# Kernel tuning notes

Measured on AMD Instinct MI355X. Metric: run time of the kernel, lower is better.

The kernel has to match this reference:

```python
import jax, jax.numpy as jnp
import numpy as np

N = 50000
E = 400000
H1, H2, D = 4, 2, 64
NEG_SLOPE = 0.2
EPS = 1e-5


def _segment_softmax(alpha, dst, num_nodes):
    # alpha: [E, H], softmax over edges sharing the same dst node
    m = jax.ops.segment_max(alpha, dst, num_segments=num_nodes)  # [N, H]
    ex = jnp.exp(alpha - m[dst])
    den = jax.ops.segment_sum(ex, dst, num_segments=num_nodes)   # [N, H]
    return ex / den[dst]


def _gat_conv(x, src, dst, eattr, W, We, a_src, a_dst, a_edge, b, heads, num_nodes):
    # x: [N, Fin] -> h: [N, H, D]; eattr: [E, Fe] -> e: [E, H, D]
    h = (x @ W).reshape(num_nodes, heads, D)
    e = (eattr @ We).reshape(-1, heads, D)
    al_src = jnp.einsum('nhd,hd->nh', h, a_src)   # [N, H]
    al_dst = jnp.einsum('nhd,hd->nh', h, a_dst)   # [N, H]
    al_e = jnp.einsum('ehd,hd->eh', e, a_edge)    # [E, H]
    alpha = al_src[src] + al_dst[dst] + al_e
    alpha = jax.nn.leaky_relu(alpha, NEG_SLOPE)
    alpha = _segment_softmax(alpha, dst, num_nodes)
    msg = h[src] * alpha[:, :, None]              # [E, H, D]
    out = jax.ops.segment_sum(msg, dst, num_segments=num_nodes)
    return out.reshape(num_nodes, heads * D) + b


def _graph_norm(x, w, b, mean_scale):
    # PyG GraphNorm over the whole (single) graph
    mean = jnp.mean(x, axis=0, keepdims=True)
    out = x - mean * mean_scale
    var = jnp.mean(out * out, axis=0, keepdims=True)
    return w * out / jnp.sqrt(var + EPS) + b


def _forward(x, edge_index, edge_attr,
             W1, We1, as1, ad1, ae1, b1, gn1_w, gn1_b, gn1_ms,
             W2, We2, as2, ad2, ae2, b2, gn2_w, gn2_b, gn2_ms,
             Wc, bc):
    # add self loops (PyG default), self-loop edge_attr = mean of edge_attr
    loops = jnp.arange(N)
    src = jnp.concatenate([edge_index[0], loops])
    dst = jnp.concatenate([edge_index[1], loops])
    ea_mean = jnp.mean(edge_attr, axis=0, keepdims=True)
    eattr = jnp.concatenate([edge_attr, jnp.broadcast_to(ea_mean, (N, edge_attr.shape[1]))])

    h = _gat_conv(x, src, dst, eattr, W1, We1, as1, ad1, ae1, b1, H1, N)
    h = jax.nn.elu(_graph_norm(h, gn1_w, gn1_b, gn1_ms))
    h = _gat_conv(h, src, dst, eattr, W2, We2, as2, ad2, ae2, b2, H2, N)
    h = jax.nn.elu(_graph_norm(h, gn2_w, gn2_b, gn2_ms))
    return h @ Wc + bc


def setup_inputs() -> dict:
    key = jax.random.key(0)
    ks = jax.random.split(key, 20)
    g = lambda k, shape, fan: jax.random.normal(k, shape, jnp.float32) * (1.0 / np.sqrt(fan))
    inp = {
        'x': jax.random.normal(ks[0], (N, 3), jnp.float32),
        'edge_index': jax.random.randint(ks[1], (2, E), 0, N),
        'edge_attr': jax.random.uniform(ks[2], (E, 2), jnp.float32),
        'W1': g(ks[3], (3, H1 * D), 3),
        'We1': g(ks[4], (2, H1 * D), 2),
        'as1': g(ks[5], (H1, D), D),
        'ad1': g(ks[6], (H1, D), D),
        'ae1': g(ks[7], (H1, D), D),
        'b1': jnp.zeros((H1 * D,), jnp.float32),
        'gn1_w': jnp.ones((H1 * D,), jnp.float32),
        'gn1_b': jnp.zeros((H1 * D,), jnp.float32),
        'gn1_ms': jnp.ones((H1 * D,), jnp.float32),
        'W2': g(ks[8], (H1 * D, H2 * D), H1 * D),
        'We2': g(ks[9], (2, H2 * D), 2),
        'as2': g(ks[10], (H2, D), D),
        'ad2': g(ks[11], (H2, D), D),
        'ae2': g(ks[12], (H2, D), D),
        'b2': jnp.zeros((H2 * D,), jnp.float32),
        'gn2_w': jnp.ones((H2 * D,), jnp.float32),
        'gn2_b': jnp.zeros((H2 * D,), jnp.float32),
        'gn2_ms': jnp.ones((H2 * D,), jnp.float32),
        # classifier 128 -> 13
        'Wc': g(ks[13], (H2 * D, 13), H2 * D),
        'bc': jnp.zeros((13,), jnp.float32),
    }
    return inp


def reference(x, edge_index, edge_attr,
              W1, We1, as1, ad1, ae1, b1, gn1_w, gn1_b, gn1_ms,
              W2, We2, as2, ad2, ae2, b2, gn2_w, gn2_b, gn2_ms,
              Wc, bc):
    return _forward(x, edge_index, edge_attr,
                    W1, We1, as1, ad1, ae1, b1, gn1_w, gn1_b, gn1_ms,
                    W2, We2, as2, ad2, ae2, b2, gn2_w, gn2_b, gn2_ms,
                    Wc, bc)
```

## Files before the change

### kernel.cpp

```cpp
#include <hip/hip_runtime.h>
#include <math.h>

#define NEG_SLOPE 0.2f
#define GEPS 1e-5f

typedef __attribute__((ext_vector_type(8))) short short8;
typedef __attribute__((ext_vector_type(4))) float floatx4;

__device__ __forceinline__ float wave_reduce_sum(float v) {
#pragma unroll
    for (int o = 32; o > 0; o >>= 1) v += __shfl_down(v, o);
    return v;
}

__device__ __forceinline__ ushort f2bf(float f) {
    union { float f; unsigned int i; } c;
    c.f = f;
    unsigned int b = c.i;
    b += 0x7fffu + ((b >> 16) & 1u);
    return (ushort)(b >> 16);
}

__device__ __forceinline__ float bf2f(ushort u) {
    union { unsigned int i; float f; } c;
    c.i = (unsigned int)u << 16;
    return c.f;
}

__device__ __forceinline__ float2 unpack_bf2(unsigned int u) {
    union { unsigned int i; float f; } a, b;
    a.i = u << 16;
    b.i = u & 0xffff0000u;
    return make_float2(a.f, b.f);
}

__device__ __forceinline__ unsigned int pack_bf2(float lo, float hi) {
    return (unsigned int)f2bf(lo) | ((unsigned int)f2bf(hi) << 16);
}

__device__ __forceinline__ float lrelu(float v) {
    return (v > 0.f) ? v : v * NEG_SLOPE;
}

__device__ __forceinline__ float elu_fast(float v) {
    return (v > 0.f) ? v : (__expf(v) - 1.f);
}

__global__ __launch_bounds__(256) void k_pre(
    const float* __restrict__ W1, const float* __restrict__ as1, const float* __restrict__ ad1,
    const float* __restrict__ ea, const int* __restrict__ dst,
    const float* __restrict__ W2, const float* __restrict__ We1,
    const float* __restrict__ ae1, const float* __restrict__ We2,
    const float* __restrict__ ae2,
    float* __restrict__ ea_sum, int* __restrict__ deg, uint4* __restrict__ Bfrag,
    float* __restrict__ C1, float* __restrict__ C2, float* __restrict__ Ps,
    float* __restrict__ Pd, int E) {
    int b = blockIdx.x;
    if (b < 16) {
        int t = b * 256 + threadIdx.x;
        int c = t >> 9, kk = (t >> 6) & 7, L = t & 63;
        int q = L >> 4, n = c * 16 + (L & 15);
        int k0 = kk * 32 + q * 8;
        unsigned int u0 = pack_bf2(W2[(k0 + 0) * 128 + n], W2[(k0 + 1) * 128 + n]);
        unsigned int u1 = pack_bf2(W2[(k0 + 2) * 128 + n], W2[(k0 + 3) * 128 + n]);
        unsigned int u2 = pack_bf2(W2[(k0 + 4) * 128 + n], W2[(k0 + 5) * 128 + n]);
        unsigned int u3 = pack_bf2(W2[(k0 + 6) * 128 + n], W2[(k0 + 7) * 128 + n]);
        Bfrag[t] = make_uint4(u0, u1, u2, u3);
        return;
    }
    if (b == 16) {
        int t = threadIdx.x, h = t >> 6, lane = t & 63;
        float p0 = We1[t] * ae1[t];
        float p1 = We1[256 + t] * ae1[t];
        p0 = wave_reduce_sum(p0);
        p1 = wave_reduce_sum(p1);
        if (lane == 0) { C1[h] = p0; C1[4 + h] = p1; }
        float av = as1[t], dv = ad1[t];
#pragma unroll
        for (int k = 0; k < 3; ++k) {
            float wv = W1[k * 256 + t];
            float ps = wave_reduce_sum(wv * av);
            float pd = wave_reduce_sum(wv * dv);
            if (lane == 0) { Ps[h * 3 + k] = ps; Pd[h * 3 + k] = pd; }
        }
        if (t < 128) {
            float q0 = We2[t] * ae2[t];
            float q1 = We2[128 + t] * ae2[t];
            q0 = wave_reduce_sum(q0);
            q1 = wave_reduce_sum(q1);
            if (lane == 0) { C2[h] = q0; C2[2 + h] = q1; }
        }
        return;
    }
    b -= 17;
    const float2* ea2 = (const float2*)ea;
    float s0 = 0.f, s1 = 0.f;
    for (int e = b * 256 + threadIdx.x; e < E; e += 256 * 256) {
        float2 v = ea2[e];
        s0 += v.x; s1 += v.y;
        atomicAdd(&deg[dst[e]], 1);
    }
    s0 = wave_reduce_sum(s0);
    s1 = wave_reduce_sum(s1);
    if ((threadIdx.x & 63) == 0) {
        atomicAdd(&ea_sum[0], s0);
        atomicAdd(&ea_sum[1], s1);
    }
}

__global__ void k_scan1(const int* __restrict__ deg, int* __restrict__ row_ptr,
                        int* __restrict__ bsum, int N) {
    __shared__ int tmp[1024];
    int tid = threadIdx.x;
    int i = blockIdx.x * 1024 + tid;
    int v = (i < N) ? deg[i] : 0;
    tmp[tid] = v;
    __syncthreads();
#pragma unroll
    for (int off = 1; off < 1024; off <<= 1) {
        int t = (tid >= off) ? tmp[tid - off] : 0;
        __syncthreads();
        tmp[tid] += t;
        __syncthreads();
    }
    if (i < N) row_ptr[i + 1] = tmp[tid];
    if (tid == 1023) bsum[blockIdx.x] = tmp[1023];
}

__global__ void k_scan23(int* __restrict__ row_ptr, const int* __restrict__ bsum,
                         const float* __restrict__ ea_sum, const float* __restrict__ C1,
                         const float* __restrict__ C2, const float* __restrict__ Ps,
                         const float* __restrict__ Pd, const float* __restrict__ x,
                         float* __restrict__ al_s1, float* __restrict__ al_d1,
                         float* __restrict__ lE1, float* __restrict__ lE2, int N, int E) {
    __shared__ int off_s;
    int t = threadIdx.x;
    if (blockIdx.x == 0 && t >= 64 && t < 68) {
        int k = t - 64;
        float m0 = ea_sum[0] / (float)E, m1 = ea_sum[1] / (float)E;
        lE1[k] = m0 * C1[k] + m1 * C1[4 + k];
        if (k < 2) lE2[k] = m0 * C2[k] + m1 * C2[2 + k];
    }
    if (t < 64) {
        int v = (t < blockIdx.x) ? bsum[t] : 0;
#pragma unroll
        for (int o = 32; o > 0; o >>= 1) v += __shfl_xor(v, o);
        if (t == 0) off_s = v;
    }
    __syncthreads();
    int off = off_s;
    int i = blockIdx.x * 1024 + t;
    if (i == 0) row_ptr[0] = 0;
    if (i < N) {
        row_ptr[i + 1] += off;
        float x0 = x[3 * i], x1 = x[3 * i + 1], x2 = x[3 * i + 2];
        float4 sv, dv;
        sv.x = fmaf(x0, Ps[0], fmaf(x1, Ps[1], x2 * Ps[2]));
        sv.y = fmaf(x0, Ps[3], fmaf(x1, Ps[4], x2 * Ps[5]));
        sv.z = fmaf(x0, Ps[6], fmaf(x1, Ps[7], x2 * Ps[8]));
        sv.w = fmaf(x0, Ps[9], fmaf(x1, Ps[10], x2 * Ps[11]));
        dv.x = fmaf(x0, Pd[0], fmaf(x1, Pd[1], x2 * Pd[2]));
        dv.y = fmaf(x0, Pd[3], fmaf(x1, Pd[4], x2 * Pd[5]));
        dv.z = fmaf(x0, Pd[6], fmaf(x1, Pd[7], x2 * Pd[8]));
        dv.w = fmaf(x0, Pd[9], fmaf(x1, Pd[10], x2 * Pd[11]));
        *(float4*)(al_s1 + 4 * (size_t)i) = sv;
        *(float4*)(al_d1 + 4 * (size_t)i) = dv;
    }
}

__global__ void k_scatfill(const int* __restrict__ dst, const int* __restrict__ src,
                           const float* __restrict__ ea, const int* __restrict__ row_ptr,
                           int* __restrict__ deg, const float* __restrict__ al_s1,
                           const float* __restrict__ al_d1, const float* __restrict__ C1,
                           float2* __restrict__ ea2, uint4* __restrict__ wmp, int E) {
    int e = blockIdx.x * 256 + threadIdx.x;
    if (e >= E) return;
    int d = dst[e];
    int r = atomicSub(&deg[d], 1);
    int slot = row_ptr[d] + r - 1;
    int s = src[e];
    float2 v = ((const float2*)ea)[e];
    float4 as = *(const float4*)(al_s1 + 4 * (size_t)s);
    float4 ad = *(const float4*)(al_d1 + 4 * (size_t)d);
    float w0 = __expf(lrelu(as.x + ad.x + v.x * C1[0] + v.y * C1[4]));
    float w1 = __expf(lrelu(as.y + ad.y + v.x * C1[1] + v.y * C1[5]));
    float w2 = __expf(lrelu(as.z + ad.z + v.x * C1[2] + v.y * C1[6]));
    float w3 = __expf(lrelu(as.w + ad.w + v.x * C1[3] + v.y * C1[7]));
    ea2[slot] = v;
    wmp[slot] = make_uint4((unsigned int)s, pack_bf2(w0, w1), pack_bf2(w2, w3), 0u);
}

__global__ __launch_bounds__(256) void k_agg1(const float* __restrict__ x,
                                              const int* __restrict__ row_ptr,
                                              const uint4* __restrict__ wmp,
                                              const float* __restrict__ al_s,
                                              const float* __restrict__ al_d,
                                              const float* __restrict__ lE,
                                              float4* __restrict__ uarr, int N) {
    int l = threadIdx.x & 31;
    int grp = threadIdx.x >> 5;
    int n = blockIdx.x * 8 + grp;
    if (n >= N) return;
    int hh = l >> 3;
    float4 asn = *(const float4*)(al_s + 4 * (size_t)n);
    float4 adn = *(const float4*)(al_d + 4 * (size_t)n);
    float ws0 = __expf(lrelu(asn.x + adn.x + lE[0]));
    float ws1 = __expf(lrelu(asn.y + adn.y + lE[1]));
    float ws2 = __expf(lrelu(asn.z + adn.z + lE[2]));
    float ws3 = __expf(lrelu(asn.w + adn.w + lE[3]));
    float z[12];
    float ds[4];
#pragma unroll
    for (int k = 0; k < 12; ++k) z[k] = 0.f;
#pragma unroll
    for (int k = 0; k < 4; ++k) ds[k] = 0.f;
    int i0 = row_ptr[n];
    int cnt = row_ptr[n + 1] - i0;
    for (int j = l; j < cnt; j += 32) {
        uint4 me = wmp[i0 + j];
        int s = (int)me.x;
        float xs0 = x[3 * s], xs1 = x[3 * s + 1], xs2 = x[3 * s + 2];
        float2 w01 = unpack_bf2(me.y);
        float2 w23 = unpack_bf2(me.z);
        z[0] = fmaf(w01.x, xs0, z[0]); z[1] = fmaf(w01.x, xs1, z[1]); z[2] = fmaf(w01.x, xs2, z[2]);
        z[3] = fmaf(w01.y, xs0, z[3]); z[4] = fmaf(w01.y, xs1, z[4]); z[5] = fmaf(w01.y, xs2, z[5]);
        z[6] = fmaf(w23.x, xs0, z[6]); z[7] = fmaf(w23.x, xs1, z[7]); z[8] = fmaf(w23.x, xs2, z[8]);
        z[9] = fmaf(w23.y, xs0, z[9]); z[10] = fmaf(w23.y, xs1, z[10]); z[11] = fmaf(w23.y, xs2, z[11]);
        ds[0] += w01.x; ds[1] += w01.y; ds[2] += w23.x; ds[3] += w23.y;
    }
    bool hi16 = (l & 16) != 0;
    float a0, a1, a2, a3, a4, a5, a6, a7, gv, rv;
    gv = hi16 ? z[0] : z[6];  rv = __shfl_xor(gv, 16); a0 = (hi16 ? z[6] : z[0]) + rv;
    gv = hi16 ? z[1] : z[7];  rv = __shfl_xor(gv, 16); a1 = (hi16 ? z[7] : z[1]) + rv;
    gv = hi16 ? z[2] : z[8];  rv = __shfl_xor(gv, 16); a2 = (hi16 ? z[8] : z[2]) + rv;
    gv = hi16 ? z[3] : z[9];  rv = __shfl_xor(gv, 16); a3 = (hi16 ? z[9] : z[3]) + rv;
    gv = hi16 ? z[4] : z[10]; rv = __shfl_xor(gv, 16); a4 = (hi16 ? z[10] : z[4]) + rv;
    gv = hi16 ? z[5] : z[11]; rv = __shfl_xor(gv, 16); a5 = (hi16 ? z[11] : z[5]) + rv;
    gv = hi16 ? ds[0] : ds[2]; rv = __shfl_xor(gv, 16); a6 = (hi16 ? ds[2] : ds[0]) + rv;
    gv = hi16 ? ds[1] : ds[3]; rv = __shfl_xor(gv, 16); a7 = (hi16 ? ds[3] : ds[1]) + rv;
    bool hi8 = (l & 8) != 0;
    float c0v, c1v, c2v, c3v;
    gv = hi8 ? a0 : a3; rv = __shfl_xor(gv, 8); c0v = (hi8 ? a3 : a0) + rv;
    gv = hi8 ? a1 : a4; rv = __shfl_xor(gv, 8); c1v = (hi8 ? a4 : a1) + rv;
    gv = hi8 ? a2 : a5; rv = __shfl_xor(gv, 8); c2v = (hi8 ? a5 : a2) + rv;
    gv = hi8 ? a6 : a7; rv = __shfl_xor(gv, 8); c3v = (hi8 ? a7 : a6) + rv;
#pragma unroll
    for (int o = 4; o > 0; o >>= 1) {
        c0v += __shfl_xor(c0v, o);
        c1v += __shfl_xor(c1v, o);
        c2v += __shfl_xor(c2v, o);
        c3v += __shfl_xor(c3v, o);
    }
    float wsh = (hh == 0) ? ws0 : (hh == 1) ? ws1 : (hh == 2) ? ws2 : ws3;
    float xn0 = x[3 * n], xn1 = x[3 * n + 1], xn2 = x[3 * n + 2];
    c0v = fmaf(wsh, xn0, c0v);
    c1v = fmaf(wsh, xn1, c1v);
    c2v = fmaf(wsh, xn2, c2v);
    c3v += wsh;
    if ((l & 7) == 0) {
        float inv = 1.f / c3v;
        uarr[(size_t)n * 4 + hh] = make_float4(c0v * inv, c1v * inv, c2v * inv, 0.f);
    }
}

__global__ __launch_bounds__(256) void k_mom(const float4* __restrict__ uarr,
                                             float* __restrict__ mom, int N4) {
    int t = threadIdx.x;
    float m[9] = {0.f, 0.f, 0.f, 0.f, 0.f, 0.f, 0.f, 0.f, 0.f};
    for (int i = blockIdx.x * 256 + t; i < N4; i += gridDim.x * 256) {
        float4 u = uarr[i];
        m[0] += u.x; m[1] += u.y; m[2] += u.z;
        m[3] = fmaf(u.x, u.x, m[3]);
        m[4] = fmaf(u.y, u.y, m[4]);
        m[5] = fmaf(u.z, u.z, m[5]);
        m[6] = fmaf(u.x, u.y, m[6]);
        m[7] = fmaf(u.x, u.z, m[7]);
        m[8] = fmaf(u.y, u.z, m[8]);
    }
    __shared__ float ls[256 * 9];
#pragma unroll
    for (int k = 0; k < 9; ++k) ls[t * 9 + k] = m[k];
    __syncthreads();
    if (t < 36) {
        int h = t / 9, k = t - h * 9;
        float s = 0.f;
        for (int tt = h; tt < 256; tt += 4) s += ls[tt * 9 + k];
        atomicAdd(&mom[t], s);
    }
}

__global__ __launch_bounds__(256) void k_gemm2_mfma(const float4* __restrict__ uarr,
                                                    const float* __restrict__ mom,
                                                    const float* __restrict__ W1,
                                                    const float* __restrict__ b1,
                                                    const float* __restrict__ gw,
                                                    const float* __restrict__ gb,
                                                    const float* __restrict__ gms,
                                                    const uint4* __restrict__ Bfrag,
                                                    const float* __restrict__ as2,
                                                    const float* __restrict__ ad2,
                                                    ushort* __restrict__ H2,
                                                    float* __restrict__ al_s,
                                                    float* __restrict__ al_d, int Nn) {
    __shared__ __align__(16) float4 Wc4[256];
    __shared__ __align__(16) float2 ABs2[256];
    __shared__ __align__(16) float4 Uld[256];
    {
        int t = threadIdx.x;
        float w0 = W1[t], w1 = W1[256 + t], w2 = W1[512 + t], bb = b1[t];
        Wc4[t] = make_float4(w0, w1, w2, bb);
        const float* mh = mom + (t >> 6) * 9;
        float invN = 1.f / (float)Nn;
        float sw = w0 * mh[0] + w1 * mh[1] + w2 * mh[2];
        float mean = fmaf(sw, invN, bb);
        float quad = w0 * w0 * mh[3] + w1 * w1 * mh[4] + w2 * w2 * mh[5] +
                     2.f * (w0 * w1 * mh[6] + w0 * w2 * mh[7] + w1 * w2 * mh[8]);
        float E2 = fmaf(fmaf(2.f * bb, sw, quad), invN, bb * bb);
        float cm = mean * gms[t];
        float var = E2 - 2.f * cm * mean + cm * cm;
        float A = gw[t] * rsqrtf(var + GEPS);
        ABs2[t] = make_float2(A, gb[t] - A * cm);
        int row = blockIdx.x * 64 + (t >> 2);
        Uld[t] = (row < Nn) ? uarr[(size_t)row * 4 + (t & 3)] : make_float4(0.f, 0.f, 0.f, 0.f);
    }
    __syncthreads();
    int wave = threadIdx.x >> 6, lane = threadIdx.x & 63;
    int q = lane >> 4, m = lane & 15;
    int rowbase = blockIdx.x * 64 + wave * 16;
    union { short8 s; unsigned int u[4]; } af[8];
#pragma unroll
    for (int kk = 0; kk < 8; ++kk) {
        float4 u = Uld[(wave * 16 + m) * 4 + (kk >> 1)];
        int c0 = kk * 32 + q * 8;
        float vv[8];
#pragma unroll
        for (int j = 0; j < 8; ++j) {
            float4 wv = Wc4[c0 + j];
            float2 ab = ABs2[c0 + j];
            float X = fmaf(u.x, wv.x, fmaf(u.y, wv.y, fmaf(u.z, wv.z, wv.w)));
            vv[j] = elu_fast(fmaf(ab.x, X, ab.y));
        }
        af[kk].u[0] = pack_bf2(vv[0], vv[1]);
        af[kk].u[1] = pack_bf2(vv[2], vv[3]);
        af[kk].u[2] = pack_bf2(vv[4], vv[5]);
        af[kk].u[3] = pack_bf2(vv[6], vv[7]);
    }
    floatx4 acc[8];
#pragma unroll
    for (int c = 0; c < 8; ++c) acc[c] = (floatx4){0.f, 0.f, 0.f, 0.f};
#pragma unroll
    for (int kk = 0; kk < 8; ++kk) {
        const uint4* bpf = Bfrag + kk * 64 + lane;
#pragma unroll
        for (int c = 0; c < 8; ++c) {
            union { short8 s; uint4 u; } bf;
            bf.u = bpf[c * 8 * 64];
            acc[c] = __builtin_amdgcn_mfma_f32_16x16x32_bf16(af[kk].s, bf.s, acc[c], 0, 0, 0);
        }
    }
    float a_s[8], a_d[8];
#pragma unroll
    for (int c = 0; c < 8; ++c) {
        a_s[c] = as2[c * 16 + m];
        a_d[c] = ad2[c * 16 + m];
    }
#pragma unroll
    for (int r = 0; r < 4; ++r) {
        int orow = rowbase + q * 4 + r;
        bool vr = orow < Nn;
        ushort us[8];
        float s0 = 0.f, s1 = 0.f, d0 = 0.f, d1 = 0.f;
#pragma unroll
        for (int c = 0; c < 8; ++c) {
            us[c] = f2bf(acc[c][r]);
            float v = bf2f(us[c]);
            if (c < 4) {
                s0 = fmaf(v, a_s[c], s0);
                d0 = fmaf(v, a_d[c], d0);
            } else {
                s1 = fmaf(v, a_s[c], s1);
                d1 = fmaf(v, a_d[c], d1);
            }
        }
#pragma unroll
        for (int o = 1; o < 16; o <<= 1) {
            s0 += __shfl_xor(s0, o);
            s1 += __shfl_xor(s1, o);
            d0 += __shfl_xor(d0, o);
            d1 += __shfl_xor(d1, o);
        }
        if (vr) {
            ushort* op = H2 + (size_t)orow * 128 + m;
#pragma unroll
            for (int c = 0; c < 8; ++c) op[c * 16] = us[c];
            if (m == 0) {
                *(float2*)(al_s + 2 * (size_t)orow) = make_float2(s0, s1);
                *(float2*)(al_d + 2 * (size_t)orow) = make_float2(d0, d1);
            }
        }
    }
}

__global__ __launch_bounds__(256) void k_agg2(const ushort* __restrict__ h2,
                                              const int* __restrict__ row_ptr,
                                              const uint4* __restrict__ wmp,
                                              const float2* __restrict__ ea2,
                                              const float* __restrict__ al_s,
                                              const float* __restrict__ al_d,
                                              const float* __restrict__ C2,
                                              const float* __restrict__ lE,
                                              const float* __restrict__ bias,
                                              ushort* __restrict__ out, int N) {
    int n = blockIdx.x * 4 + (threadIdx.x >> 6);
    if (n >= N) return;
    int lane = threadIdx.x & 63;
    int g = lane >> 4, c16 = lane & 15;
    bool hi = c16 >= 8;
    const uint4* h2u4 = (const uint4*)h2;
    float2 ad = *(const float2*)(al_d + 2 * (size_t)n);
    float2 as = *(const float2*)(al_s + 2 * (size_t)n);
    float wsA = __expf(lrelu(as.x + ad.x + lE[0]));
    float wsB = __expf(lrelu(as.y + ad.y + lE[1]));
    float c2x = hi ? C2[1] : C2[0];
    float c2y = hi ? C2[3] : C2[2];
    float adh = hi ? ad.y : ad.x;
    uint4 hs = h2u4[(size_t)n * 16 + c16];
    float wself = (g == 0) ? (hi ? wsB : wsA) : 0.f;
    float dsum = wself;
    float acc[8];
    {
        float2 t0 = unpack_bf2(hs.x), t1 = unpack_bf2(hs.y);
        float2 t2 = unpack_bf2(hs.z), t3 = unpack_bf2(hs.w);
        acc[0] = wself * t0.x; acc[1] = wself * t0.y;
        acc[2] = wself * t1.x; acc[3] = wself * t1.y;
        acc[4] = wself * t2.x; acc[5] = wself * t2.y;
        acc[6] = wself * t3.x; acc[7] = wself * t3.y;
    }
    int i0 = row_ptr[n];
    int cnt = row_ptr[n + 1] - i0;
    if (cnt > 0) {
        int last = cnt - 1;
        int nit = (cnt + 3) >> 2;
        int j0 = g;      float mkA = 1.f; if (j0 > last) { j0 = last; mkA = 0.f; }
        int j1 = 4 + g;  float mkB = 1.f; if (j1 > last) { j1 = last; mkB = 0.f; }
        int j2 = 8 + g;  float mkC = 1.f; if (j2 > last) { j2 = last; mkC = 0.f; }
        int j3 = 12 + g; float mkD = 1.f; if (j3 > last) { j3 = last; mkD = 0.f; }
        uint4 meA = wmp[i0 + j0]; float2 eaA = ea2[i0 + j0];
        uint4 meB = wmp[i0 + j1]; float2 eaB = ea2[i0 + j1];
        uint4 meC = wmp[i0 + j2]; float2 eaC = ea2[i0 + j2];
        uint4 meD = wmp[i0 + j3]; float2 eaD = ea2[i0 + j3];
        float2 alA = *(const float2*)(al_s + 2 * (size_t)meA.x);
        uint4 gvA = h2u4[(size_t)meA.x * 16 + c16];
        float2 alB = *(const float2*)(al_s + 2 * (size_t)meB.x);
        uint4 gvB = h2u4[(size_t)meB.x * 16 + c16];
        float2 alC = *(const float2*)(al_s + 2 * (size_t)meC.x);
        uint4 gvC = h2u4[(size_t)meC.x * 16 + c16];
        for (int it = 0; it < nit - 1; ++it) {
            float2 alD = *(const float2*)(al_s + 2 * (size_t)meD.x);
            uint4 gvD = h2u4[(size_t)meD.x * 16 + c16];
            int jn = 4 * (it + 4) + g;
            float mn = 1.f;
            if (jn > last) { jn = last; mn = 0.f; }
            uint4 meE = wmp[i0 + jn]; float2 eaE = ea2[i0 + jn];
            float lg = (hi ? alA.y : alA.x) + adh + eaA.x * c2x + eaA.y * c2y;
            float wg = __expf(lrelu(lg)) * mkA;
            dsum += wg;
            float2 u;
            u = unpack_bf2(gvA.x); acc[0] = fmaf(wg, u.x, acc[0]); acc[1] = fmaf(wg, u.y, acc[1]);
            u = unpack_bf2(gvA.y); acc[2] = fmaf(wg, u.x, acc[2]); acc[3] = fmaf(wg, u.y, acc[3]);
            u = unpack_bf2(gvA.z); acc[4] = fmaf(wg, u.x, acc[4]); acc[5] = fmaf(wg, u.y, acc[5]);
            u = unpack_bf2(gvA.w); acc[6] = fmaf(wg, u.x, acc[6]); acc[7] = fmaf(wg, u.y, acc[7]);
            meA = meB; meB = meC; meC = meD; meD = meE;
            eaA = eaB; eaB = eaC; eaC = eaD; eaD = eaE;
            alA = alB; alB = alC; alC = alD;
            gvA = gvB; gvB = gvC; gvC = gvD;
            mkA = mkB; mkB = mkC; mkC = mkD; mkD = mn;
        }
        float lg = (hi ? alA.y : alA.x) + adh + eaA.x * c2x + eaA.y * c2y;
        float wg = __expf(lrelu(lg)) * mkA;
        dsum += wg;
        float2 u;
        u = unpack_bf2(gvA.x); acc[0] = fmaf(wg, u.x, acc[0]); acc[1] = fmaf(wg, u.y, acc[1]);
        u = unpack_bf2(gvA.y); acc[2] = fmaf(wg, u.x, acc[2]); acc[3] = fmaf(wg, u.y, acc[3]);
        u = unpack_bf2(gvA.z); acc[4] = fmaf(wg, u.x, acc[4]); acc[5] = fmaf(wg, u.y, acc[5]);
        u = unpack_bf2(gvA.w); acc[6] = fmaf(wg, u.x, acc[6]); acc[7] = fmaf(wg, u.y, acc[7]);
    }
#pragma unroll
    for (int k = 0; k < 8; ++k) {
        acc[k] += __shfl_xor(acc[k], 16);
        acc[k] += __shfl_xor(acc[k], 32);
    }
    dsum += __shfl_xor(dsum, 16);
    dsum += __shfl_xor(dsum, 32);
    if (g == 0) {
        float inv = 1.f / dsum;
        const float* bp = bias + c16 * 8;
        float4 b0 = *(const float4*)bp;
        float4 b1 = *(const float4*)(bp + 4);
        uint4 o;
        o.x = pack_bf2(fmaf(acc[0], inv, b0.x), fmaf(acc[1], inv, b0.y));
        o.y = pack_bf2(fmaf(acc[2], inv, b0.z), fmaf(acc[3], inv, b0.w));
        o.z = pack_bf2(fmaf(acc[4], inv, b1.x), fmaf(acc[5], inv, b1.y));
        o.w = pack_bf2(fmaf(acc[6], inv, b1.z), fmaf(acc[7], inv, b1.w));
        ((uint4*)out)[(size_t)n * 16 + c16] = o;
    }
}

template <int C4>
__global__ __launch_bounds__(256) void k_stats_bf(const ushort* __restrict__ x,
                                                  float* __restrict__ stats, int rows) {
    const int C = C4 * 8;
    const int RG = 256 / C4;
    int t = threadIdx.x;
    int c = t & (C4 - 1);
    int rg = t / C4;
    int rpb = (rows + gridDim.x - 1) / gridDim.x;
    int r0 = blockIdx.x * rpb;
    int r1 = r0 + rpb;
    if (r1 > rows) r1 = rows;
    const uint4* xu = (const uint4*)x;
    float s[8] = {0.f, 0.f, 0.f, 0.f, 0.f, 0.f, 0.f, 0.f};
    float q[8] = {0.f, 0.f, 0.f, 0.f, 0.f, 0.f, 0.f, 0.f};
    for (int r = r0 + rg; r < r1; r += RG) {
        uint4 v = xu[(size_t)r * C4 + c];
        float2 a0 = unpack_bf2(v.x), a1 = unpack_bf2(v.y);
        float2 a2 = unpack_bf2(v.z), a3 = unpack_bf2(v.w);
        s[0] += a0.x; q[0] = fmaf(a0.x, a0.x, q[0]);
        s[1] += a0.y; q[1] = fmaf(a0.y, a0.y, q[1]);
        s[2] += a1.x; q[2] = fmaf(a1.x, a1.x, q[2]);
        s[3] += a1.y; q[3] = fmaf(a1.y, a1.y, q[3]);
        s[4] += a2.x; q[4] = fmaf(a2.x, a2.x, q[4]);
        s[5] += a2.y; q[5] = fmaf(a2.y, a2.y, q[5]);
        s[6] += a3.x; q[6] = fmaf(a3.x, a3.x, q[6]);
        s[7] += a3.y; q[7] = fmaf(a3.y, a3.y, q[7]);
    }
    __shared__ float ls[256 * 16];
#pragma unroll
    for (int k = 0; k < 8; ++k) {
        ls[t * 16 + k] = s[k];
        ls[t * 16 + 8 + k] = q[k];
    }
    __syncthreads();
    if (t < C) {
        int cc = t >> 3, k = t & 7;
        float ssum = 0.f, qsum = 0.f;
#pragma unroll
        for (int g = 0; g < RG; ++g) {
            ssum += ls[(g * C4 + cc) * 16 + k];
            qsum += ls[(g * C4 + cc) * 16 + 8 + k];
        }
        atomicAdd(&stats[t], ssum);
        atomicAdd(&stats[C + t], qsum);
    }
}

__global__ __launch_bounds__(256) void k_cls(const ushort* __restrict__ X,
                                             const float* __restrict__ stats,
                                             const float* __restrict__ gw,
                                             const float* __restrict__ gb,
                                             const float* __restrict__ gms,
                                             const float* __restrict__ Wc,
                                             const float* __restrict__ bc,
                                             float* __restrict__ out, int Nn) {
    __shared__ __align__(16) float ls[16 * 132];
    __shared__ __align__(16) float wT[13 * 132];
    __shared__ __align__(16) float ABs[256];
    __shared__ float bS[13];
    int t = threadIdx.x;
    int n0 = blockIdx.x * 16;
    if (t < 128) {
        float inv = 1.f / (float)Nn;
        float mean = stats[t] * inv;
        float cm = mean * gms[t];
        float var = stats[128 + t] * inv - 2.f * cm * mean + cm * cm;
        float A = gw[t] * rsqrtf(var + GEPS);
        ABs[t] = A;
        ABs[128 + t] = gb[t] - A * cm;
    }
    for (int i = t; i < 128 * 13; i += 256) {
        int k = i / 13, j = i - k * 13;
        wT[j * 132 + k] = Wc[i];
    }
    if (t < 13) bS[t] = bc[t];
    __syncthreads();
    const unsigned int* xu = (const unsigned int*)X;
    for (int idx = t; idx < 16 * 64; idx += 256) {
        int r = idx >> 6, ku = idx & 63;
        int row = n0 + r;
        float vx = 0.f, vy = 0.f;
        if (row < Nn) {
            float2 v = unpack_bf2(xu[(size_t)row * 64 + ku]);
            int k = 2 * ku;
            vx = elu_fast(fmaf(ABs[k], v.x, ABs[128 + k]));
            vy = elu_fast(fmaf(ABs[k + 1], v.y, ABs[128 + k + 1]));
        }
        ls[r * 132 + 2 * ku] = vx;
        ls[r * 132 + 2 * ku + 1] = vy;
    }
    __syncthreads();
    if (t < 208) {
        int r = t / 13, j = t - r * 13;
        int row = n0 + r;
        if (row < Nn) {
            float acc = bS[j];
            const float* lr = &ls[r * 132];
            const float* wr = &wT[j * 132];
#pragma unroll 8
            for (int k = 0; k < 128; k += 4) {
                float4 a = *(const float4*)&lr[k];
                float4 b = *(const float4*)&wr[k];
                acc = fmaf(a.x, b.x, fmaf(a.y, b.y, fmaf(a.z, b.z, fmaf(a.w, b.w, acc))));
            }
            out[(size_t)row * 13 + j] = acc;
        }
    }
}

extern "C" void kernel_launch(void* const* d_in, const int* in_sizes, int n_in, void* d_out,
                              int out_size, void* d_ws, size_t ws_size, hipStream_t stream) {
    const float* x = (const float*)d_in[0];
    const int* edge_index = (const int*)d_in[1];
    const float* edge_attr = (const float*)d_in[2];
    const float* W1 = (const float*)d_in[3];
    const float* We1 = (const float*)d_in[4];
    const float* as1 = (const float*)d_in[5];
    const float* ad1 = (const float*)d_in[6];
    const float* ae1 = (const float*)d_in[7];
    const float* b1 = (const float*)d_in[8];
    const float* gn1_w = (const float*)d_in[9];
    const float* gn1_b = (const float*)d_in[10];
    const float* gn1_ms = (const float*)d_in[11];
    const float* W2 = (const float*)d_in[12];
    const float* We2 = (const float*)d_in[13];
    const float* as2 = (const float*)d_in[14];
    const float* ad2 = (const float*)d_in[15];
    const float* ae2 = (const float*)d_in[16];
    const float* b2 = (const float*)d_in[17];
    const float* gn2_w = (const float*)d_in[18];
    const float* gn2_b = (const float*)d_in[19];
    const float* gn2_ms = (const float*)d_in[20];
    const float* Wc = (const float*)d_in[21];
    const float* bc = (const float*)d_in[22];

    const int N = in_sizes[0] / 3;
    const int E = in_sizes[1] / 2;
    const int* srcv = edge_index;
    const int* dstv = edge_index + E;

    char* w = (char*)d_ws;
    auto carveB = [&](size_t bytes) -> void* {
        void* p = (void*)w;
        w += ((bytes + 255) / 256) * 256;
        return p;
    };
    int* deg = (int*)carveB((size_t)N * 4);
    float* ea_sum = (float*)carveB(8);
    float* mom = (float*)carveB(36 * 4);
    float* statsB = (float*)carveB(256 * 4);
    char* zero_end = w;
    int* row_ptr = (int*)carveB((size_t)(N + 1) * 4);
    int* bsum = (int*)carveB(1024 * 4);
    float2* ea2 = (float2*)carveB((size_t)E * 8);
    uint4* wmp = (uint4*)carveB((size_t)E * 16);
    float* C1 = (float*)carveB(8 * 4);
    float* C2 = (float*)carveB(4 * 4);
    float* Ps = (float*)carveB(12 * 4);
    float* Pd = (float*)carveB(12 * 4);
    float* lE1 = (float*)carveB(4 * 4);
    float* lE2 = (float*)carveB(2 * 4);
    uint4* Bfrag = (uint4*)carveB(4096 * 16);
    float* al_s1 = (float*)carveB((size_t)N * 4 * 4);
    float* al_d1 = (float*)carveB((size_t)N * 4 * 4);
    float* al_s2 = (float*)carveB((size_t)N * 2 * 4);
    float* al_d2 = (float*)carveB((size_t)N * 2 * 4);
    float4* uarr = (float4*)carveB((size_t)N * 4 * 16);
    ushort* h2b = (ushort*)carveB((size_t)N * 128 * 2);
    ushort* out2b = (ushort*)carveB((size_t)N * 128 * 2);

    hipMemsetAsync(deg, 0, (size_t)(zero_end - (char*)deg), stream);

    const int nb1 = (N + 1023) / 1024;
    const int ebl = (E + 255) / 256;

    k_pre<<<17 + 256, 256, 0, stream>>>(W1, as1, ad1, edge_attr, dstv, W2, We1, ae1, We2, ae2,
                                        ea_sum, deg, Bfrag, C1, C2, Ps, Pd, E);
    k_scan1<<<nb1, 1024, 0, stream>>>(deg, row_ptr, bsum, N);
    k_scan23<<<nb1, 1024, 0, stream>>>(row_ptr, bsum, ea_sum, C1, C2, Ps, Pd, x, al_s1, al_d1,
                                       lE1, lE2, N, E);
    k_scatfill<<<ebl, 256, 0, stream>>>(dstv, srcv, edge_attr, row_ptr, deg, al_s1, al_d1, C1,
                                        ea2, wmp, E);
    k_agg1<<<(N + 7) / 8, 256, 0, stream>>>(x, row_ptr, wmp, al_s1, al_d1, lE1, uarr, N);
    k_mom<<<128, 256, 0, stream>>>(uarr, mom, N * 4);
    k_gemm2_mfma<<<(N + 63) / 64, 256, 0, stream>>>(uarr, mom, W1, b1, gn1_w, gn1_b, gn1_ms,
                                                    Bfrag, as2, ad2, h2b, al_s2, al_d2, N);
    k_agg2<<<(N + 3) / 4, 256, 0, stream>>>(h2b, row_ptr, wmp, ea2, al_s2, al_d2, C2, lE2, b2,
                                            out2b, N);
    k_stats_bf<16><<<256, 256, 0, stream>>>(out2b, statsB, N);
    k_cls<<<(N + 15) / 16, 256, 0, stream>>>(out2b, statsB, gn2_w, gn2_b, gn2_ms, Wc, bc,
                                             (float*)d_out, N);
}
```

Measured before the change: 265.8 us.

## Move layer-1 edge weight computation from scatter into aggregation, merge edge arrays

The scatter kernel now writes only a packed float4 per edge (source index plus edge attributes) instead of computing exp attention weights and writing separate bf16 weight and edge-attr arrays. Layer-1 aggregation recomputes the weights from a new interleaved per-node record holding x and the source logits, read with one gather. Layer 2 reads the single merged edge array too. This cuts scatter traffic and removes one edge stream, at the cost of extra gathers and exp work inside agg1.

```diff
diff --git a/kernel.cpp b/kernel.cpp
--- a/kernel.cpp
+++ b/kernel.cpp
@@ -131,7 +131,7 @@
                          const float* __restrict__ ea_sum, const float* __restrict__ C1,
                          const float* __restrict__ C2, const float* __restrict__ Ps,
                          const float* __restrict__ Pd, const float* __restrict__ x,
-                         float* __restrict__ al_s1, float* __restrict__ al_d1,
+                         float4* __restrict__ ndr, float* __restrict__ al_d1,
                          float* __restrict__ lE1, float* __restrict__ lE2, int N, int E) {
     __shared__ int off_s;
     int t = threadIdx.x;
@@ -163,38 +163,29 @@
         dv.y = fmaf(x0, Pd[3], fmaf(x1, Pd[4], x2 * Pd[5]));
         dv.z = fmaf(x0, Pd[6], fmaf(x1, Pd[7], x2 * Pd[8]));
         dv.w = fmaf(x0, Pd[9], fmaf(x1, Pd[10], x2 * Pd[11]));
-        *(float4*)(al_s1 + 4 * (size_t)i) = sv;
+        ndr[2 * (size_t)i] = make_float4(x0, x1, x2, 0.f);
+        ndr[2 * (size_t)i + 1] = sv;
         *(float4*)(al_d1 + 4 * (size_t)i) = dv;
     }
 }
 
-__global__ void k_scatfill(const int* __restrict__ dst, const int* __restrict__ src,
-                           const float* __restrict__ ea, const int* __restrict__ row_ptr,
-                           int* __restrict__ deg, const float* __restrict__ al_s1,
-                           const float* __restrict__ al_d1, const float* __restrict__ C1,
-                           float2* __restrict__ ea2, uint4* __restrict__ wmp, int E) {
+__global__ void k_scat(const int* __restrict__ dst, const int* __restrict__ src,
+                       const float* __restrict__ ea, const int* __restrict__ row_ptr,
+                       int* __restrict__ deg, float4* __restrict__ ed4, int E) {
     int e = blockIdx.x * 256 + threadIdx.x;
     if (e >= E) return;
     int d = dst[e];
     int r = atomicSub(&deg[d], 1);
     int slot = row_ptr[d] + r - 1;
-    int s = src[e];
     float2 v = ((const float2*)ea)[e];
-    float4 as = *(const float4*)(al_s1 + 4 * (size_t)s);
-    float4 ad = *(const float4*)(al_d1 + 4 * (size_t)d);
-    float w0 = __expf(lrelu(as.x + ad.x + v.x * C1[0] + v.y * C1[4]));
-    float w1 = __expf(lrelu(as.y + ad.y + v.x * C1[1] + v.y * C1[5]));
-    float w2 = __expf(lrelu(as.z + ad.z + v.x * C1[2] + v.y * C1[6]));
-    float w3 = __expf(lrelu(as.w + ad.w + v.x * C1[3] + v.y * C1[7]));
-    ea2[slot] = v;
-    wmp[slot] = make_uint4((unsigned int)s, pack_bf2(w0, w1), pack_bf2(w2, w3), 0u);
-}
-
-__global__ __launch_bounds__(256) void k_agg1(const float* __restrict__ x,
+    ed4[slot] = make_float4(__int_as_float(src[e]), v.x, v.y, 0.f);
+}
+
+__global__ __launch_bounds__(256) void k_agg1(const float4* __restrict__ ndr,
                                               const int* __restrict__ row_ptr,
-                                              const uint4* __restrict__ wmp,
-                                              const float* __restrict__ al_s,
+                                              const float4* __restrict__ ed4,
                                               const float* __restrict__ al_d,
+                                              const float* __restrict__ C1,
                                               const float* __restrict__ lE,
                                               float4* __restrict__ uarr, int N) {
     int l = threadIdx.x & 31;
@@ -202,12 +193,15 @@
     int n = blockIdx.x * 8 + grp;
     if (n >= N) return;
     int hh = l >> 3;
-    float4 asn = *(const float4*)(al_s + 4 * (size_t)n);
     float4 adn = *(const float4*)(al_d + 4 * (size_t)n);
-    float ws0 = __expf(lrelu(asn.x + adn.x + lE[0]));
-    float ws1 = __expf(lrelu(asn.y + adn.y + lE[1]));
-    float ws2 = __expf(lrelu(asn.z + adn.z + lE[2]));
-    float ws3 = __expf(lrelu(asn.w + adn.w + lE[3]));
+    float4 c1a = *(const float4*)C1;
+    float4 c1b = *(const float4*)(C1 + 4);
+    float4 ndx = ndr[2 * (size_t)n];
+    float4 nas = ndr[2 * (size_t)n + 1];
+    float ws0 = __expf(lrelu(nas.x + adn.x + lE[0]));
+    float ws1 = __expf(lrelu(nas.y + adn.y + lE[1]));
+    float ws2 = __expf(lrelu(nas.z + adn.z + lE[2]));
+    float ws3 = __expf(lrelu(nas.w + adn.w + lE[3]));
     float z[12];
     float ds[4];
 #pragma unroll
@@ -217,16 +211,19 @@
     int i0 = row_ptr[n];
     int cnt = row_ptr[n + 1] - i0;
     for (int j = l; j < cnt; j += 32) {
-        uint4 me = wmp[i0 + j];
-        int s = (int)me.x;
-        float xs0 = x[3 * s], xs1 = x[3 * s + 1], xs2 = x[3 * s + 2];
-        float2 w01 = unpack_bf2(me.y);
-        float2 w23 = unpack_bf2(me.z);
-        z[0] = fmaf(w01.x, xs0, z[0]); z[1] = fmaf(w01.x, xs1, z[1]); z[2] = fmaf(w01.x, xs2, z[2]);
-        z[3] = fmaf(w01.y, xs0, z[3]); z[4] = fmaf(w01.y, xs1, z[4]); z[5] = fmaf(w01.y, xs2, z[5]);
-        z[6] = fmaf(w23.x, xs0, z[6]); z[7] = fmaf(w23.x, xs1, z[7]); z[8] = fmaf(w23.x, xs2, z[8]);
-        z[9] = fmaf(w23.y, xs0, z[9]); z[10] = fmaf(w23.y, xs1, z[10]); z[11] = fmaf(w23.y, xs2, z[11]);
-        ds[0] += w01.x; ds[1] += w01.y; ds[2] += w23.x; ds[3] += w23.y;
+        float4 m = ed4[i0 + j];
+        int s = __float_as_int(m.x);
+        float4 xr = ndr[2 * (size_t)s];
+        float4 as = ndr[2 * (size_t)s + 1];
+        float w0 = __expf(lrelu(as.x + adn.x + m.y * c1a.x + m.z * c1b.x));
+        float w1 = __expf(lrelu(as.y + adn.y + m.y * c1a.y + m.z * c1b.y));
+        float w2 = __expf(lrelu(as.z + adn.z + m.y * c1a.z + m.z * c1b.z));
+        float w3 = __expf(lrelu(as.w + adn.w + m.y * c1a.w + m.z * c1b.w));
+        z[0] = fmaf(w0, xr.x, z[0]); z[1] = fmaf(w0, xr.y, z[1]); z[2] = fmaf(w0, xr.z, z[2]);
+        z[3] = fmaf(w1, xr.x, z[3]); z[4] = fmaf(w1, xr.y, z[4]); z[5] = fmaf(w1, xr.z, z[5]);
+        z[6] = fmaf(w2, xr.x, z[6]); z[7] = fmaf(w2, xr.y, z[7]); z[8] = fmaf(w2, xr.z, z[8]);
+        z[9] = fmaf(w3, xr.x, z[9]); z[10] = fmaf(w3, xr.y, z[10]); z[11] = fmaf(w3, xr.z, z[11]);
+        ds[0] += w0; ds[1] += w1; ds[2] += w2; ds[3] += w3;
     }
     bool hi16 = (l & 16) != 0;
     float a0, a1, a2, a3, a4, a5, a6, a7, gv, rv;
@@ -252,10 +249,9 @@
         c3v += __shfl_xor(c3v, o);
     }
     float wsh = (hh == 0) ? ws0 : (hh == 1) ? ws1 : (hh == 2) ? ws2 : ws3;
-    float xn0 = x[3 * n], xn1 = x[3 * n + 1], xn2 = x[3 * n + 2];
-    c0v = fmaf(wsh, xn0, c0v);
-    c1v = fmaf(wsh, xn1, c1v);
-    c2v = fmaf(wsh, xn2, c2v);
+    c0v = fmaf(wsh, ndx.x, c0v);
+    c1v = fmaf(wsh, ndx.y, c1v);
+    c2v = fmaf(wsh, ndx.z, c2v);
     c3v += wsh;
     if ((l & 7) == 0) {
         float inv = 1.f / c3v;
@@ -403,8 +399,7 @@
 
 __global__ __launch_bounds__(256) void k_agg2(const ushort* __restrict__ h2,
                                               const int* __restrict__ row_ptr,
-                                              const uint4* __restrict__ wmp,
-                                              const float2* __restrict__ ea2,
+                                              const float4* __restrict__ ed4,
                                               const float* __restrict__ al_s,
                                               const float* __restrict__ al_d,
                                               const float* __restrict__ C2,
@@ -445,24 +440,28 @@
         int j1 = 4 + g;  float mkB = 1.f; if (j1 > last) { j1 = last; mkB = 0.f; }
         int j2 = 8 + g;  float mkC = 1.f; if (j2 > last) { j2 = last; mkC = 0.f; }
         int j3 = 12 + g; float mkD = 1.f; if (j3 > last) { j3 = last; mkD = 0.f; }
-        uint4 meA = wmp[i0 + j0]; float2 eaA = ea2[i0 + j0];
-        uint4 meB = wmp[i0 + j1]; float2 eaB = ea2[i0 + j1];
-        uint4 meC = wmp[i0 + j2]; float2 eaC = ea2[i0 + j2];
-        uint4 meD = wmp[i0 + j3]; float2 eaD = ea2[i0 + j3];
-        float2 alA = *(const float2*)(al_s + 2 * (size_t)meA.x);
-        uint4 gvA = h2u4[(size_t)meA.x * 16 + c16];
-        float2 alB = *(const float2*)(al_s + 2 * (size_t)meB.x);
-        uint4 gvB = h2u4[(size_t)meB.x * 16 + c16];
-        float2 alC = *(const float2*)(al_s + 2 * (size_t)meC.x);
-        uint4 gvC = h2u4[(size_t)meC.x * 16 + c16];
+        float4 mA = ed4[i0 + j0];
+        float4 mB = ed4[i0 + j1];
+        float4 mC = ed4[i0 + j2];
+        float4 mD = ed4[i0 + j3];
+        int sA = __float_as_int(mA.x);
+        float2 alA = *(const float2*)(al_s + 2 * (size_t)sA);
+        uint4 gvA = h2u4[(size_t)sA * 16 + c16];
+        int sB = __float_as_int(mB.x);
+        float2 alB = *(const float2*)(al_s + 2 * (size_t)sB);
+        uint4 gvB = h2u4[(size_t)sB * 16 + c16];
+        int sC = __float_as_int(mC.x);
+        float2 alC = *(const float2*)(al_s + 2 * (size_t)sC);
+        uint4 gvC = h2u4[(size_t)sC * 16 + c16];
         for (int it = 0; it < nit - 1; ++it) {
-            float2 alD = *(const float2*)(al_s + 2 * (size_t)meD.x);
-            uint4 gvD = h2u4[(size_t)meD.x * 16 + c16];
+            int sD = __float_as_int(mD.x);
+            float2 alD = *(const float2*)(al_s + 2 * (size_t)sD);
+            uint4 gvD = h2u4[(size_t)sD * 16 + c16];
             int jn = 4 * (it + 4) + g;
             float mn = 1.f;
             if (jn > last) { jn = last; mn = 0.f; }
-            uint4 meE = wmp[i0 + jn]; float2 eaE = ea2[i0 + jn];
-            float lg = (hi ? alA.y : alA.x) + adh + eaA.x * c2x + eaA.y * c2y;
+            float4 mE = ed4[i0 + jn];
+            float lg = (hi ? alA.y : alA.x) + adh + mA.y * c2x + mA.z * c2y;
             float wg = __expf(lrelu(lg)) * mkA;
             dsum += wg;
             float2 u;
@@ -470,13 +469,12 @@
             u = unpack_bf2(gvA.y); acc[2] = fmaf(wg, u.x, acc[2]); acc[3] = fmaf(wg, u.y, acc[3]);
             u = unpack_bf2(gvA.z); acc[4] = fmaf(wg, u.x, acc[4]); acc[5] = fmaf(wg, u.y, acc[5]);
             u = unpack_bf2(gvA.w); acc[6] = fmaf(wg, u.x, acc[6]); acc[7] = fmaf(wg, u.y, acc[7]);
-            meA = meB; meB = meC; meC = meD; meD = meE;
-            eaA = eaB; eaB = eaC; eaC = eaD; eaD = eaE;
+            mA = mB; mB = mC; mC = mD; mD = mE;
             alA = alB; alB = alC; alC = alD;
             gvA = gvB; gvB = gvC; gvC = gvD;
             mkA = mkB; mkB = mkC; mkC = mkD; mkD = mn;
         }
-        float lg = (hi ? alA.y : alA.x) + adh + eaA.x * c2x + eaA.y * c2y;
+        float lg = (hi ? alA.y : alA.x) + adh + mA.y * c2x + mA.z * c2y;
         float wg = __expf(lrelu(lg)) * mkA;
         dsum += wg;
         float2 u;
@@ -660,8 +658,7 @@
     char* zero_end = w;
     int* row_ptr = (int*)carveB((size_t)(N + 1) * 4);
     int* bsum = (int*)carveB(1024 * 4);
-    float2* ea2 = (float2*)carveB((size_t)E * 8);
-    uint4* wmp = (uint4*)carveB((size_t)E * 16);
+    float4* ed4 = (float4*)carveB((size_t)E * 16);
     float* C1 = (float*)carveB(8 * 4);
     float* C2 = (float*)carveB(4 * 4);
     float* Ps = (float*)carveB(12 * 4);
@@ -669,7 +666,7 @@
     float* lE1 = (float*)carveB(4 * 4);
     float* lE2 = (float*)carveB(2 * 4);
     uint4* Bfrag = (uint4*)carveB(4096 * 16);
-    float* al_s1 = (float*)carveB((size_t)N * 4 * 4);
+    float4* ndr = (float4*)carveB((size_t)N * 32);
     float* al_d1 = (float*)carveB((size_t)N * 4 * 4);
     float* al_s2 = (float*)carveB((size_t)N * 2 * 4);
     float* al_d2 = (float*)carveB((size_t)N * 2 * 4);
@@ -685,15 +682,14 @@
     k_pre<<<17 + 256, 256, 0, stream>>>(W1, as1, ad1, edge_attr, dstv, W2, We1, ae1, We2, ae2,
                                         ea_sum, deg, Bfrag, C1, C2, Ps, Pd, E);
     k_scan1<<<nb1, 1024, 0, stream>>>(deg, row_ptr, bsum, N);
-    k_scan23<<<nb1, 1024, 0, stream>>>(row_ptr, bsum, ea_sum, C1, C2, Ps, Pd, x, al_s1, al_d1,
+    k_scan23<<<nb1, 1024, 0, stream>>>(row_ptr, bsum, ea_sum, C1, C2, Ps, Pd, x, ndr, al_d1,
                                        lE1, lE2, N, E);
-    k_scatfill<<<ebl, 256, 0, stream>>>(dstv, srcv, edge_attr, row_ptr, deg, al_s1, al_d1, C1,
-                                        ea2, wmp, E);
-    k_agg1<<<(N + 7) / 8, 256, 0, stream>>>(x, row_ptr, wmp, al_s1, al_d1, lE1, uarr, N);
+    k_scat<<<ebl, 256, 0, stream>>>(dstv, srcv, edge_attr, row_ptr, deg, ed4, E);
+    k_agg1<<<(N + 7) / 8, 256, 0, stream>>>(ndr, row_ptr, ed4, al_d1, C1, lE1, uarr, N);
     k_mom<<<128, 256, 0, stream>>>(uarr, mom, N * 4);
     k_gemm2_mfma<<<(N + 63) / 64, 256, 0, stream>>>(uarr, mom, W1, b1, gn1_w, gn1_b, gn1_ms,
                                                     Bfrag, as2, ad2, h2b, al_s2, al_d2, N);
-    k_agg2<<<(N + 3) / 4, 256, 0, stream>>>(h2b, row_ptr, wmp, ea2, al_s2, al_d2, C2, lE2, b2,
+    k_agg2<<<(N + 3) / 4, 256, 0, stream>>>(h2b, row_ptr, ed4, al_s2, al_d2, C2, lE2, b2,
                                             out2b, N);
     k_stats_bf<16><<<256, 256, 0, stream>>>(out2b, statsB, N);
     k_cls<<<(N + 15) / 16, 256, 0, stream>>>(out2b, statsB, gn2_w, gn2_b, gn2_ms, Wc, bc,
```

Result: no change. 268.2 us (+0.9%).
